# Performance work log

Measured on AMD Instinct MI355X. Metric: run time of the kernel, lower is better.

The kernel has to match this reference:

```python
import jax, jax.numpy as jnp
import numpy as np

N_USERS = 8192
N_ITEMS = 4096
BATCH = 8192


def setup_inputs() -> dict:
    key = jax.random.key(0)
    k1, k2, k3, k4, k5, k6, k7 = jax.random.split(key, 7)
    # ratings in {0..5}; zeros mark unrated entries (needed for nonzero masking)
    rating_mtx = jax.random.randint(k1, (N_USERS, N_ITEMS), 0, 6).astype(jnp.float32)
    user = jax.random.randint(k2, (BATCH,), 0, N_USERS)
    item = jax.random.randint(k3, (BATCH,), 0, N_ITEMS)
    # learned parameters (xavier-normal similarity; biases initialized like global mean)
    xavier_std = float(np.sqrt(2.0 / (N_USERS + N_USERS)))
    user_similarity = jax.random.normal(k4, (N_USERS, N_USERS), dtype=jnp.float32) * xavier_std
    user_bias = jax.random.normal(k5, (N_USERS,), dtype=jnp.float32)
    item_bias = jax.random.normal(k6, (N_ITEMS,), dtype=jnp.float32)
    global_bias = jax.random.normal(k7, (), dtype=jnp.float32)
    return {
        "user": user,
        "item": item,
        "rating_mtx": rating_mtx,
        "user_similarity": user_similarity,
        "user_bias": user_bias,
        "item_bias": item_bias,
        "global_bias": global_bias,
    }


def reference(user, item, rating_mtx, user_similarity, user_bias, item_bias, global_bias):
    # per-user mean over NONZERO ratings (0 if user rated nothing) -- single fused
    # masked sum/count reduction replacing the per-row python loop
    mask = rating_mtx != 0  # [U, I]
    cnt = jnp.sum(mask, axis=1)  # [U]
    row_sum = jnp.sum(rating_mtx, axis=1)  # zeros contribute nothing
    user_bias_fixed = jnp.where(cnt > 0, row_sum / jnp.maximum(cnt, 1).astype(rating_mtx.dtype), 0.0)

    adjusted = rating_mtx - user_bias_fixed[:, None]  # [U, I]
    similarities = user_similarity[user]  # [B, U]
    item_ratings = adjusted[:, item]  # [U, B]
    user_scores = jnp.sum(similarities * item_ratings.T, axis=1)  # [B]

    bias = user_bias[user] + item_bias[item] + global_bias  # [B]
    return jax.nn.sigmoid(user_scores + bias) * 5.0
```

## Files before the change

kernel.cpp:

```cpp
#include <hip/hip_runtime.h>
#include <math.h>

#define N_USERS 8192
#define N_ITEMS 4096
#define BATCH   8192
#define NTILE_I (N_ITEMS / 64)

__global__ __launch_bounds__(256) void k_trans(const float* __restrict__ R,
                                               unsigned char* __restrict__ AT,
                                               float* __restrict__ psum,
                                               float* __restrict__ pcnt) {
    __shared__ float lds[64][65];
    const int colBase = blockIdx.x * 64;
    const int rowBase = blockIdx.y * 64;
    const int tx = threadIdx.x, ty = threadIdx.y;
    const int x4 = tx * 4;

    float s[4], c[4];
    #pragma unroll
    for (int k = 0; k < 4; ++k) {
        const int y = ty + 16 * k;
        float4 v = *(const float4*)(R + (size_t)(rowBase + y) * N_ITEMS + colBase + x4);
        lds[y][x4 + 0] = v.x;
        lds[y][x4 + 1] = v.y;
        lds[y][x4 + 2] = v.z;
        lds[y][x4 + 3] = v.w;
        s[k] = v.x + v.y + v.z + v.w;
        c[k] = (v.x != 0.f) + (v.y != 0.f) + (v.z != 0.f) + (v.w != 0.f);
    }
    #pragma unroll
    for (int k = 0; k < 4; ++k) {
        #pragma unroll
        for (int off = 8; off; off >>= 1) {
            s[k] += __shfl_down(s[k], off, 16);
            c[k] += __shfl_down(c[k], off, 16);
        }
    }
    if (tx == 0) {
        #pragma unroll
        for (int k = 0; k < 4; ++k) {
            const int u = rowBase + ty + 16 * k;
            psum[(size_t)blockIdx.x * N_USERS + u] = s[k];
            pcnt[(size_t)blockIdx.x * N_USERS + u] = c[k];
        }
    }
    __syncthreads();

    const int tid = ty * 16 + tx;
    const int il = tid >> 2;
    const int ch = tid & 3;
    union { unsigned char b[16]; int4 v; } w;
    #pragma unroll
    for (int e = 0; e < 16; ++e) {
        w.b[e] = (unsigned char)(int)lds[ch * 16 + e][il];
    }
    *(int4*)(AT + (size_t)(colBase + il) * N_USERS + rowBase + ch * 16) = w.v;
}

__global__ __launch_bounds__(256) void k_fin(const float* __restrict__ psum,
                                             const float* __restrict__ pcnt,
                                             float* __restrict__ ub) {
    __shared__ float ss[4][64], sc[4][64];
    const int ul  = threadIdx.x & 63;
    const int seg = threadIdx.x >> 6;
    const int u = blockIdx.x * 64 + ul;
    float s = 0.f, c = 0.f;
    #pragma unroll
    for (int k = 0; k < 16; ++k) {
        const int t = seg * 16 + k;
        s += psum[(size_t)t * N_USERS + u];
        c += pcnt[(size_t)t * N_USERS + u];
    }
    ss[seg][ul] = s;
    sc[seg][ul] = c;
    __syncthreads();
    if (seg == 0) {
        s = ss[0][ul] + ss[1][ul] + ss[2][ul] + ss[3][ul];
        c = sc[0][ul] + sc[1][ul] + sc[2][ul] + sc[3][ul];
        ub[u] = (c > 0.f) ? s / fmaxf(c, 1.f) : 0.f;
    }
}

__global__ __launch_bounds__(512, 6) void k_main(const float* __restrict__ S,
                                                 const unsigned char* __restrict__ AT,
                                                 const float* __restrict__ ub,
                                                 const int* __restrict__ user,
                                                 const int* __restrict__ item,
                                                 const float* __restrict__ ubias,
                                                 const float* __restrict__ ibias,
                                                 const float* __restrict__ gbias,
                                                 float* __restrict__ out) {
    __shared__ float4 ubs[N_USERS / 4];
    #pragma unroll
    for (int t = 0; t < 4; ++t) {
        ubs[t * 512 + threadIdx.x] = ((const float4*)ub)[t * 512 + threadIdx.x];
    }
    __syncthreads();

    const int wave = threadIdx.x >> 6;
    const int lane = threadIdx.x & 63;
    const int b = blockIdx.x * 8 + wave;
    const int su = user[b];
    const int j  = item[b];
    const float4* srow = (const float4*)(S + (size_t)su * N_USERS);
    const uint2*  arow = (const uint2*)(AT + (size_t)j * N_USERS);

    float acc = 0.f;
    #pragma unroll 4
    for (int i = 0; i < 16; ++i) {
        const int idx = i * 64 + lane;
        uint2  a  = arow[idx];
        float4 s0 = srow[2 * idx + 0];
        float4 s1 = srow[2 * idx + 1];
        float4 u0 = ubs[2 * idx + 0];
        float4 u1 = ubs[2 * idx + 1];
        acc += s0.x * ((float)( a.x        & 0xffu) - u0.x);
        acc += s0.y * ((float)((a.x >>  8) & 0xffu) - u0.y);
        acc += s0.z * ((float)((a.x >> 16) & 0xffu) - u0.z);
        acc += s0.w * ((float)( a.x >> 24         ) - u0.w);
        acc += s1.x * ((float)( a.y        & 0xffu) - u1.x);
        acc += s1.y * ((float)((a.y >>  8) & 0xffu) - u1.y);
        acc += s1.z * ((float)((a.y >> 16) & 0xffu) - u1.z);
        acc += s1.w * ((float)( a.y >> 24         ) - u1.w);
    }
    #pragma unroll
    for (int off = 32; off; off >>= 1) acc += __shfl_down(acc, off);

    if (lane == 0) {
        float score = acc + ubias[su] + ibias[j] + gbias[0];
        out[b] = 5.f / (1.f + expf(-score));
    }
}

__global__ __launch_bounds__(256) void k_ubfix(const float* __restrict__ R,
                                               float* __restrict__ ub) {
    const int wave = threadIdx.x >> 6;
    const int lane = threadIdx.x & 63;
    const int u = blockIdx.x * 4 + wave;
    const float4* row4 = (const float4*)(R + (size_t)u * N_ITEMS);
    float s = 0.f, c = 0.f;
    #pragma unroll
    for (int i = 0; i < 16; ++i) {
        float4 v = row4[i * 64 + lane];
        s += v.x + v.y + v.z + v.w;
        c += (v.x != 0.f) + (v.y != 0.f) + (v.z != 0.f) + (v.w != 0.f);
    }
    #pragma unroll
    for (int off = 32; off; off >>= 1) {
        s += __shfl_down(s, off);
        c += __shfl_down(c, off);
    }
    if (lane == 0)
        ub[u] = (c > 0.f) ? s / fmaxf(c, 1.f) : 0.f;
}

__global__ __launch_bounds__(256) void k_direct(const float* __restrict__ S,
                                                const float* __restrict__ R,
                                                const float* __restrict__ ub,
                                                const int* __restrict__ user,
                                                const int* __restrict__ item,
                                                const float* __restrict__ ubias,
                                                const float* __restrict__ ibias,
                                                const float* __restrict__ gbias,
                                                float* __restrict__ out) {
    const int b = blockIdx.x;
    const int su = user[b];
    const int j  = item[b];
    const float* srow = S + (size_t)su * N_USERS;
    float acc = 0.f;
    for (int u = threadIdx.x; u < N_USERS; u += 256) {
        acc += srow[u] * (R[(size_t)u * N_ITEMS + j] - ub[u]);
    }
    for (int off = 32; off; off >>= 1) acc += __shfl_down(acc, off);
    __shared__ float sa[4];
    const int lane = threadIdx.x & 63, w = threadIdx.x >> 6;
    if (lane == 0) sa[w] = acc;
    __syncthreads();
    if (threadIdx.x == 0) {
        float score = sa[0] + sa[1] + sa[2] + sa[3]
                    + ubias[su] + ibias[j] + gbias[0];
        out[b] = 5.f / (1.f + expf(-score));
    }
}

extern "C" void kernel_launch(void* const* d_in, const int* in_sizes, int n_in,
                              void* d_out, int out_size, void* d_ws, size_t ws_size,
                              hipStream_t stream) {
    const int*   user  = (const int*)d_in[0];
    const int*   item  = (const int*)d_in[1];
    const float* R     = (const float*)d_in[2];
    const float* S     = (const float*)d_in[3];
    const float* ubias = (const float*)d_in[4];
    const float* ibias = (const float*)d_in[5];
    const float* gbias = (const float*)d_in[6];
    float* out = (float*)d_out;

    float* ub   = (float*)d_ws;
    float* psum = (float*)((char*)d_ws + (64u << 10));
    float* pcnt = (float*)((char*)d_ws + (64u << 10) + ((size_t)NTILE_I * N_USERS * 4));
    unsigned char* AT = (unsigned char*)((char*)d_ws + (8u << 20));
    const size_t need = (8u << 20) + (size_t)N_ITEMS * N_USERS;

    if (ws_size >= need) {
        dim3 tgrid(NTILE_I, N_USERS / 64);
        dim3 tblk(16, 16);
        k_trans<<<tgrid, tblk, 0, stream>>>(R, AT, psum, pcnt);
        k_fin<<<N_USERS / 64, 256, 0, stream>>>(psum, pcnt, ub);
        k_main<<<BATCH / 8, 512, 0, stream>>>(S, AT, ub, user, item, ubias, ibias, gbias, out);
    } else {
        k_ubfix<<<N_USERS / 4, 256, 0, stream>>>(R, ub);
        k_direct<<<BATCH, 256, 0, stream>>>(S, R, ub, user, item, ubias, ibias, gbias, out);
    }
}
```

Before: 442.9 us.

## Fuse transpose, bias finalize and main dot into persistent kernel with grid barriers

Replaces three kernel launches with one persistent kernel of 512 blocks that run the transpose/quantize phase, the per-user mean finalize and the gather-dot phase, separated by software grid barriers built on global atomics. The barrier counter is zeroed with a memset before launch. The aim is to remove launch gaps and tail effects between the stages. In exchange, the kernel relies on all 512 blocks being co-resident, since otherwise the spin barrier can deadlock. The barriers also serialize the phases, and larger 128x64 transpose tiles raise LDS use per block.

New measurement: 628.1 us. 41.8% more time.

```diff
diff --git a/kernel.cpp b/kernel.cpp
--- a/kernel.cpp
+++ b/kernel.cpp
@@ -4,131 +4,172 @@
 #define N_USERS 8192
 #define N_ITEMS 4096
 #define BATCH   8192
-#define NTILE_I (N_ITEMS / 64)
-
-__global__ __launch_bounds__(256) void k_trans(const float* __restrict__ R,
-                                               unsigned char* __restrict__ AT,
-                                               float* __restrict__ psum,
-                                               float* __restrict__ pcnt) {
-    __shared__ float lds[64][65];
-    const int colBase = blockIdx.x * 64;
-    const int rowBase = blockIdx.y * 64;
-    const int tx = threadIdx.x, ty = threadIdx.y;
-    const int x4 = tx * 4;
-
-    float s[4], c[4];
-    #pragma unroll
-    for (int k = 0; k < 4; ++k) {
-        const int y = ty + 16 * k;
-        float4 v = *(const float4*)(R + (size_t)(rowBase + y) * N_ITEMS + colBase + x4);
-        lds[y][x4 + 0] = v.x;
-        lds[y][x4 + 1] = v.y;
-        lds[y][x4 + 2] = v.z;
-        lds[y][x4 + 3] = v.w;
-        s[k] = v.x + v.y + v.z + v.w;
-        c[k] = (v.x != 0.f) + (v.y != 0.f) + (v.z != 0.f) + (v.w != 0.f);
-    }
-    #pragma unroll
-    for (int k = 0; k < 4; ++k) {
+#define NTILE_I 64
+#define NTILE_U2 64
+#define NTILES  (NTILE_I * NTILE_U2)
+#define FGRID   512
+#define FTHR    512
+
+union SMem {
+    float  tr[128][65];
+    float4 ubs[N_USERS / 4];
+    struct { float ss[8][64]; float sc[8][64]; } fin;
+};
+
+__device__ __forceinline__ void gridbar(unsigned* bar, unsigned nblk) {
+    __syncthreads();
+    if (threadIdx.x == 0) {
+        __threadfence();
+        unsigned g = __hip_atomic_load(&bar[1], __ATOMIC_RELAXED, __HIP_MEMORY_SCOPE_AGENT);
+        unsigned a = __hip_atomic_fetch_add(&bar[0], 1u, __ATOMIC_ACQ_REL, __HIP_MEMORY_SCOPE_AGENT) + 1;
+        if (a == nblk) {
+            __hip_atomic_store(&bar[0], 0u, __ATOMIC_RELAXED, __HIP_MEMORY_SCOPE_AGENT);
+            __hip_atomic_store(&bar[1], g + 1u, __ATOMIC_RELEASE, __HIP_MEMORY_SCOPE_AGENT);
+        } else {
+            while (__hip_atomic_load(&bar[1], __ATOMIC_ACQUIRE, __HIP_MEMORY_SCOPE_AGENT) == g) {
+                __builtin_amdgcn_s_sleep(2);
+            }
+        }
+        __threadfence();
+    }
+    __syncthreads();
+}
+
+__global__ __launch_bounds__(FTHR, 4) void k_fused(const float* __restrict__ R,
+                                                   unsigned char* __restrict__ AT,
+                                                   float* __restrict__ psum,
+                                                   float* __restrict__ pcnt,
+                                                   float* __restrict__ ub,
+                                                   unsigned* __restrict__ bar,
+                                                   const float* __restrict__ S,
+                                                   const int* __restrict__ user,
+                                                   const int* __restrict__ item,
+                                                   const float* __restrict__ ubias,
+                                                   const float* __restrict__ ibias,
+                                                   const float* __restrict__ gbias,
+                                                   float* __restrict__ out) {
+    __shared__ SMem sm;
+    const int tid = threadIdx.x;
+    const int blk = blockIdx.x;
+
+    {
+        const int tx = tid & 15;
+        const int ty = tid >> 4;
+        const int x4 = tx * 4;
+        for (int it = 0; it < 8; ++it) {
+            const int t = blk * 8 + it;
+            const int bx = t & 63;
+            const int by = t >> 6;
+            const int colBase = bx * 64;
+            const int rowBase = by * 128;
+
+            float s[4], c[4];
+            #pragma unroll
+            for (int k = 0; k < 4; ++k) {
+                const int y = ty + 32 * k;
+                float4 v = *(const float4*)(R + (size_t)(rowBase + y) * N_ITEMS + colBase + x4);
+                sm.tr[y][x4 + 0] = v.x;
+                sm.tr[y][x4 + 1] = v.y;
+                sm.tr[y][x4 + 2] = v.z;
+                sm.tr[y][x4 + 3] = v.w;
+                s[k] = v.x + v.y + v.z + v.w;
+                c[k] = (v.x != 0.f) + (v.y != 0.f) + (v.z != 0.f) + (v.w != 0.f);
+            }
+            #pragma unroll
+            for (int k = 0; k < 4; ++k) {
+                #pragma unroll
+                for (int off = 8; off; off >>= 1) {
+                    s[k] += __shfl_down(s[k], off, 16);
+                    c[k] += __shfl_down(c[k], off, 16);
+                }
+            }
+            if (tx == 0) {
+                #pragma unroll
+                for (int k = 0; k < 4; ++k) {
+                    const int u = rowBase + ty + 32 * k;
+                    psum[(size_t)bx * N_USERS + u] = s[k];
+                    pcnt[(size_t)bx * N_USERS + u] = c[k];
+                }
+            }
+            __syncthreads();
+
+            const int il = tid >> 3;
+            const int ch = tid & 7;
+            union { unsigned char b[16]; int4 v; } w;
+            #pragma unroll
+            for (int e = 0; e < 16; ++e) {
+                w.b[e] = (unsigned char)(int)sm.tr[ch * 16 + e][il];
+            }
+            *(int4*)(AT + (size_t)(colBase + il) * N_USERS + rowBase + ch * 16) = w.v;
+            __syncthreads();
+        }
+    }
+    gridbar(bar, FGRID);
+
+    if (blk < 128) {
+        const int ul  = tid & 63;
+        const int seg = tid >> 6;
+        const int u = blk * 64 + ul;
+        float s = 0.f, c = 0.f;
         #pragma unroll
-        for (int off = 8; off; off >>= 1) {
-            s[k] += __shfl_down(s[k], off, 16);
-            c[k] += __shfl_down(c[k], off, 16);
-        }
-    }
-    if (tx == 0) {
+        for (int k = 0; k < 8; ++k) {
+            const int t = seg * 8 + k;
+            s += psum[(size_t)t * N_USERS + u];
+            c += pcnt[(size_t)t * N_USERS + u];
+        }
+        sm.fin.ss[seg][ul] = s;
+        sm.fin.sc[seg][ul] = c;
+        __syncthreads();
+        if (tid < 64) {
+            s = 0.f; c = 0.f;
+            #pragma unroll
+            for (int k = 0; k < 8; ++k) { s += sm.fin.ss[k][ul]; c += sm.fin.sc[k][ul]; }
+            ub[u] = (c > 0.f) ? s / fmaxf(c, 1.f) : 0.f;
+        }
+    }
+    gridbar(bar, FGRID);
+
+    #pragma unroll
+    for (int t = 0; t < 4; ++t) {
+        sm.ubs[t * FTHR + tid] = ((const float4*)ub)[t * FTHR + tid];
+    }
+    __syncthreads();
+
+    const int wave = tid >> 6;
+    const int lane = tid & 63;
+    #pragma unroll
+    for (int g = 0; g < 2; ++g) {
+        const int b = (blk * 2 + g) * 8 + wave;
+        const int su = user[b];
+        const int j  = item[b];
+        const float4* srow = (const float4*)(S + (size_t)su * N_USERS);
+        const uint2*  arow = (const uint2*)(AT + (size_t)j * N_USERS);
+
+        float acc = 0.f;
+        #pragma unroll 4
+        for (int i = 0; i < 16; ++i) {
+            const int idx = i * 64 + lane;
+            uint2  a  = arow[idx];
+            float4 s0 = srow[2 * idx + 0];
+            float4 s1 = srow[2 * idx + 1];
+            float4 u0 = sm.ubs[2 * idx + 0];
+            float4 u1 = sm.ubs[2 * idx + 1];
+            acc += s0.x * ((float)( a.x        & 0xffu) - u0.x);
+            acc += s0.y * ((float)((a.x >>  8) & 0xffu) - u0.y);
+            acc += s0.z * ((float)((a.x >> 16) & 0xffu) - u0.z);
+            acc += s0.w * ((float)( a.x >> 24         ) - u0.w);
+            acc += s1.x * ((float)( a.y        & 0xffu) - u1.x);
+            acc += s1.y * ((float)((a.y >>  8) & 0xffu) - u1.y);
+            acc += s1.z * ((float)((a.y >> 16) & 0xffu) - u1.z);
+            acc += s1.w * ((float)( a.y >> 24         ) - u1.w);
+        }
         #pragma unroll
-        for (int k = 0; k < 4; ++k) {
-            const int u = rowBase + ty + 16 * k;
-            psum[(size_t)blockIdx.x * N_USERS + u] = s[k];
-            pcnt[(size_t)blockIdx.x * N_USERS + u] = c[k];
-        }
-    }
-    __syncthreads();
-
-    const int tid = ty * 16 + tx;
-    const int il = tid >> 2;
-    const int ch = tid & 3;
-    union { unsigned char b[16]; int4 v; } w;
-    #pragma unroll
-    for (int e = 0; e < 16; ++e) {
-        w.b[e] = (unsigned char)(int)lds[ch * 16 + e][il];
-    }
-    *(int4*)(AT + (size_t)(colBase + il) * N_USERS + rowBase + ch * 16) = w.v;
-}
-
-__global__ __launch_bounds__(256) void k_fin(const float* __restrict__ psum,
-                                             const float* __restrict__ pcnt,
-                                             float* __restrict__ ub) {
-    __shared__ float ss[4][64], sc[4][64];
-    const int ul  = threadIdx.x & 63;
-    const int seg = threadIdx.x >> 6;
-    const int u = blockIdx.x * 64 + ul;
-    float s = 0.f, c = 0.f;
-    #pragma unroll
-    for (int k = 0; k < 16; ++k) {
-        const int t = seg * 16 + k;
-        s += psum[(size_t)t * N_USERS + u];
-        c += pcnt[(size_t)t * N_USERS + u];
-    }
-    ss[seg][ul] = s;
-    sc[seg][ul] = c;
-    __syncthreads();
-    if (seg == 0) {
-        s = ss[0][ul] + ss[1][ul] + ss[2][ul] + ss[3][ul];
-        c = sc[0][ul] + sc[1][ul] + sc[2][ul] + sc[3][ul];
-        ub[u] = (c > 0.f) ? s / fmaxf(c, 1.f) : 0.f;
-    }
-}
-
-__global__ __launch_bounds__(512, 6) void k_main(const float* __restrict__ S,
-                                                 const unsigned char* __restrict__ AT,
-                                                 const float* __restrict__ ub,
-                                                 const int* __restrict__ user,
-                                                 const int* __restrict__ item,
-                                                 const float* __restrict__ ubias,
-                                                 const float* __restrict__ ibias,
-                                                 const float* __restrict__ gbias,
-                                                 float* __restrict__ out) {
-    __shared__ float4 ubs[N_USERS / 4];
-    #pragma unroll
-    for (int t = 0; t < 4; ++t) {
-        ubs[t * 512 + threadIdx.x] = ((const float4*)ub)[t * 512 + threadIdx.x];
-    }
-    __syncthreads();
-
-    const int wave = threadIdx.x >> 6;
-    const int lane = threadIdx.x & 63;
-    const int b = blockIdx.x * 8 + wave;
-    const int su = user[b];
-    const int j  = item[b];
-    const float4* srow = (const float4*)(S + (size_t)su * N_USERS);
-    const uint2*  arow = (const uint2*)(AT + (size_t)j * N_USERS);
-
-    float acc = 0.f;
-    #pragma unroll 4
-    for (int i = 0; i < 16; ++i) {
-        const int idx = i * 64 + lane;
-        uint2  a  = arow[idx];
-        float4 s0 = srow[2 * idx + 0];
-        float4 s1 = srow[2 * idx + 1];
-        float4 u0 = ubs[2 * idx + 0];
-        float4 u1 = ubs[2 * idx + 1];
-        acc += s0.x * ((float)( a.x        & 0xffu) - u0.x);
-        acc += s0.y * ((float)((a.x >>  8) & 0xffu) - u0.y);
-        acc += s0.z * ((float)((a.x >> 16) & 0xffu) - u0.z);
-        acc += s0.w * ((float)( a.x >> 24         ) - u0.w);
-        acc += s1.x * ((float)( a.y        & 0xffu) - u1.x);
-        acc += s1.y * ((float)((a.y >>  8) & 0xffu) - u1.y);
-        acc += s1.z * ((float)((a.y >> 16) & 0xffu) - u1.z);
-        acc += s1.w * ((float)( a.y >> 24         ) - u1.w);
-    }
-    #pragma unroll
-    for (int off = 32; off; off >>= 1) acc += __shfl_down(acc, off);
-
-    if (lane == 0) {
-        float score = acc + ubias[su] + ibias[j] + gbias[0];
-        out[b] = 5.f / (1.f + expf(-score));
+        for (int off = 32; off; off >>= 1) acc += __shfl_down(acc, off);
+
+        if (lane == 0) {
+            float score = acc + ubias[su] + ibias[j] + gbias[0];
+            out[b] = 5.f / (1.f + expf(-score));
+        }
     }
 }
 
@@ -195,18 +236,17 @@
     const float* gbias = (const float*)d_in[6];
     float* out = (float*)d_out;
 
-    float* ub   = (float*)d_ws;
-    float* psum = (float*)((char*)d_ws + (64u << 10));
-    float* pcnt = (float*)((char*)d_ws + (64u << 10) + ((size_t)NTILE_I * N_USERS * 4));
+    float* ub       = (float*)d_ws;
+    unsigned* bar   = (unsigned*)((char*)d_ws + (48u << 10));
+    float* psum     = (float*)((char*)d_ws + (64u << 10));
+    float* pcnt     = (float*)((char*)d_ws + (64u << 10) + (size_t)64 * N_USERS * 4);
     unsigned char* AT = (unsigned char*)((char*)d_ws + (8u << 20));
     const size_t need = (8u << 20) + (size_t)N_ITEMS * N_USERS;
 
     if (ws_size >= need) {
-        dim3 tgrid(NTILE_I, N_USERS / 64);
-        dim3 tblk(16, 16);
-        k_trans<<<tgrid, tblk, 0, stream>>>(R, AT, psum, pcnt);
-        k_fin<<<N_USERS / 64, 256, 0, stream>>>(psum, pcnt, ub);
-        k_main<<<BATCH / 8, 512, 0, stream>>>(S, AT, ub, user, item, ubias, ibias, gbias, out);
+        hipMemsetAsync(bar, 0, 16, stream);
+        k_fused<<<FGRID, FTHR, 0, stream>>>(R, AT, psum, pcnt, ub, bar,
+                                            S, user, item, ubias, ibias, gbias, out);
     } else {
         k_ubfix<<<N_USERS / 4, 256, 0, stream>>>(R, ub);
         k_direct<<<BATCH, 256, 0, stream>>>(S, R, ub, user, item, ubias, ibias, gbias, out);
```

## Replace partial-sum finalize kernel with atomics and fold mean into main kernel

Applied to the files above, without the earlier changes.

The transpose kernel now uses 128-row tiles with 512 threads and accumulates per-user sums and nonzero counts straight into global arrays with atomicAdd. This removes the partial-sum buffers and the separate finalize kernel. The main kernel computes each user mean from sum and count while staging it into LDS. It adds a memset of the accumulators and atomic contention (64 column tiles per user), and float atomics make the sum order nondeterministic.

Result: slower. 452.0 us (+2.0%).

```diff
diff --git a/kernel.cpp b/kernel.cpp
--- a/kernel.cpp
+++ b/kernel.cpp
@@ -4,27 +4,28 @@
 #define N_USERS 8192
 #define N_ITEMS 4096
 #define BATCH   8192
-#define NTILE_I (N_ITEMS / 64)
 
-__global__ __launch_bounds__(256) void k_trans(const float* __restrict__ R,
+__global__ __launch_bounds__(512) void k_trans(const float* __restrict__ R,
                                                unsigned char* __restrict__ AT,
-                                               float* __restrict__ psum,
-                                               float* __restrict__ pcnt) {
-    __shared__ float lds[64][65];
+                                               float* __restrict__ gsum,
+                                               float* __restrict__ gcnt) {
+    __shared__ float tr[128][65];
     const int colBase = blockIdx.x * 64;
-    const int rowBase = blockIdx.y * 64;
-    const int tx = threadIdx.x, ty = threadIdx.y;
+    const int rowBase = blockIdx.y * 128;
+    const int tid = threadIdx.x;
+    const int tx = tid & 15;
+    const int ty = tid >> 4;
     const int x4 = tx * 4;
 
     float s[4], c[4];
     #pragma unroll
     for (int k = 0; k < 4; ++k) {
-        const int y = ty + 16 * k;
+        const int y = ty + 32 * k;
         float4 v = *(const float4*)(R + (size_t)(rowBase + y) * N_ITEMS + colBase + x4);
-        lds[y][x4 + 0] = v.x;
-        lds[y][x4 + 1] = v.y;
-        lds[y][x4 + 2] = v.z;
-        lds[y][x4 + 3] = v.w;
+        tr[y][x4 + 0] = v.x;
+        tr[y][x4 + 1] = v.y;
+        tr[y][x4 + 2] = v.z;
+        tr[y][x4 + 3] = v.w;
         s[k] = v.x + v.y + v.z + v.w;
         c[k] = (v.x != 0.f) + (v.y != 0.f) + (v.z != 0.f) + (v.w != 0.f);
     }
@@ -39,51 +40,27 @@
     if (tx == 0) {
         #pragma unroll
         for (int k = 0; k < 4; ++k) {
-            const int u = rowBase + ty + 16 * k;
-            psum[(size_t)blockIdx.x * N_USERS + u] = s[k];
-            pcnt[(size_t)blockIdx.x * N_USERS + u] = c[k];
+            const int u = rowBase + ty + 32 * k;
+            atomicAdd(&gsum[u], s[k]);
+            atomicAdd(&gcnt[u], c[k]);
         }
     }
     __syncthreads();
 
-    const int tid = ty * 16 + tx;
-    const int il = tid >> 2;
-    const int ch = tid & 3;
+    const int il = tid >> 3;
+    const int ch = tid & 7;
     union { unsigned char b[16]; int4 v; } w;
     #pragma unroll
     for (int e = 0; e < 16; ++e) {
-        w.b[e] = (unsigned char)(int)lds[ch * 16 + e][il];
+        w.b[e] = (unsigned char)(int)tr[ch * 16 + e][il];
     }
     *(int4*)(AT + (size_t)(colBase + il) * N_USERS + rowBase + ch * 16) = w.v;
 }
 
-__global__ __launch_bounds__(256) void k_fin(const float* __restrict__ psum,
-                                             const float* __restrict__ pcnt,
-                                             float* __restrict__ ub) {
-    __shared__ float ss[4][64], sc[4][64];
-    const int ul  = threadIdx.x & 63;
-    const int seg = threadIdx.x >> 6;
-    const int u = blockIdx.x * 64 + ul;
-    float s = 0.f, c = 0.f;
-    #pragma unroll
-    for (int k = 0; k < 16; ++k) {
-        const int t = seg * 16 + k;
-        s += psum[(size_t)t * N_USERS + u];
-        c += pcnt[(size_t)t * N_USERS + u];
-    }
-    ss[seg][ul] = s;
-    sc[seg][ul] = c;
-    __syncthreads();
-    if (seg == 0) {
-        s = ss[0][ul] + ss[1][ul] + ss[2][ul] + ss[3][ul];
-        c = sc[0][ul] + sc[1][ul] + sc[2][ul] + sc[3][ul];
-        ub[u] = (c > 0.f) ? s / fmaxf(c, 1.f) : 0.f;
-    }
-}
-
 __global__ __launch_bounds__(512, 6) void k_main(const float* __restrict__ S,
                                                  const unsigned char* __restrict__ AT,
-                                                 const float* __restrict__ ub,
+                                                 const float* __restrict__ gsum,
+                                                 const float* __restrict__ gcnt,
                                                  const int* __restrict__ user,
                                                  const int* __restrict__ item,
                                                  const float* __restrict__ ubias,
@@ -93,7 +70,15 @@
     __shared__ float4 ubs[N_USERS / 4];
     #pragma unroll
     for (int t = 0; t < 4; ++t) {
-        ubs[t * 512 + threadIdx.x] = ((const float4*)ub)[t * 512 + threadIdx.x];
+        const int p = t * 512 + threadIdx.x;
+        float4 sv = ((const float4*)gsum)[p];
+        float4 cv = ((const float4*)gcnt)[p];
+        float4 u;
+        u.x = (cv.x > 0.f) ? sv.x / cv.x : 0.f;
+        u.y = (cv.y > 0.f) ? sv.y / cv.y : 0.f;
+        u.z = (cv.z > 0.f) ? sv.z / cv.z : 0.f;
+        u.w = (cv.w > 0.f) ? sv.w / cv.w : 0.f;
+        ubs[p] = u;
     }
     __syncthreads();
 
@@ -195,19 +180,19 @@
     const float* gbias = (const float*)d_in[6];
     float* out = (float*)d_out;
 
-    float* ub   = (float*)d_ws;
-    float* psum = (float*)((char*)d_ws + (64u << 10));
-    float* pcnt = (float*)((char*)d_ws + (64u << 10) + ((size_t)NTILE_I * N_USERS * 4));
+    float* gsum = (float*)d_ws;
+    float* gcnt = (float*)((char*)d_ws + (32u << 10));
     unsigned char* AT = (unsigned char*)((char*)d_ws + (8u << 20));
     const size_t need = (8u << 20) + (size_t)N_ITEMS * N_USERS;
 
     if (ws_size >= need) {
-        dim3 tgrid(NTILE_I, N_USERS / 64);
-        dim3 tblk(16, 16);
-        k_trans<<<tgrid, tblk, 0, stream>>>(R, AT, psum, pcnt);
-        k_fin<<<N_USERS / 64, 256, 0, stream>>>(psum, pcnt, ub);
-        k_main<<<BATCH / 8, 512, 0, stream>>>(S, AT, ub, user, item, ubias, ibias, gbias, out);
+        hipMemsetAsync(d_ws, 0, 64u << 10, stream);
+        dim3 tgrid(N_ITEMS / 64, N_USERS / 128);
+        k_trans<<<tgrid, 512, 0, stream>>>(R, AT, gsum, gcnt);
+        k_main<<<BATCH / 8, 512, 0, stream>>>(S, AT, gsum, gcnt,
+                                              user, item, ubias, ibias, gbias, out);
     } else {
+        float* ub = (float*)d_ws;
         k_ubfix<<<N_USERS / 4, 256, 0, stream>>>(R, ub);
         k_direct<<<BATCH, 256, 0, stream>>>(S, R, ub, user, item, ubias, ibias, gbias, out);
     }
```
